# Kernel optimization log

Hardware: AMD Instinct MI355X
Metric: run time of the kernel (lower is better)

## Reference

```python
import jax, jax.numpy as jnp
import numpy as np

BATCH = 4096
INPUT_SIZE = 8192
IO = 16            # inputoutput_dim
D_STATE = 32       # statespace_dim
N_STAGES = INPUT_SIZE // IO  # 512


def _glorot(key, shape):
    # glorot-uniform over the trailing matrix dims, matching get_random_glorot_uniform_matrix
    lim = float(np.sqrt(6.0 / (shape[-2] + shape[-1])))
    return jax.random.uniform(key, shape, minval=-lim, maxval=lim, dtype=jnp.float32)


def setup_inputs() -> dict:
    key = jax.random.key(0)
    ks = jax.random.split(key, 10)
    U = jax.random.normal(ks[0], (BATCH, INPUT_SIZE), dtype=jnp.float32)
    A = _glorot(ks[1], (N_STAGES, D_STATE, D_STATE))
    B = _glorot(ks[2], (N_STAGES, D_STATE, IO))
    C = _glorot(ks[3], (N_STAGES, IO, D_STATE))
    D = _glorot(ks[4], (N_STAGES, IO, IO))
    E = _glorot(ks[5], (N_STAGES, D_STATE, D_STATE))
    F = _glorot(ks[6], (N_STAGES, D_STATE, IO))
    G = _glorot(ks[7], (N_STAGES, IO, D_STATE))
    lim_b = float(np.sqrt(6.0 / INPUT_SIZE))
    bias = jax.random.uniform(ks[8], (INPUT_SIZE,), minval=-lim_b, maxval=lim_b, dtype=jnp.float32)
    return {"U": U, "A": A, "B": B, "C": C, "D": D, "E": E, "F": F, "G": G, "bias": bias}


def reference(U, A, B, C, D, E, F, G, bias):
    bt, p = U.shape
    n, io, d = C.shape
    u = U.reshape(bt, n, io).transpose(1, 0, 2)  # (N, batch, io)
    x0 = jnp.zeros((bt, d), dtype=U.dtype)

    # causal: y_k = C_k x_k + D_k u_k ; x_{k+1} = A_k x_k + B_k u_k, x_0 = 0
    def causal_step(x, inp):
        A_k, B_k, C_k, D_k, u_k = inp
        y_k = x @ C_k.T + u_k @ D_k.T
        x = x @ A_k.T + u_k @ B_k.T
        return x, y_k

    _, y_c = jax.lax.scan(causal_step, x0, (A, B, C, D, u))

    # anticausal (runs from last stage to first): y_k += G_k z_k ; z_{k-1} = E_k z_k + F_k u_k, z_N = 0
    def anti_step(z, inp):
        E_k, F_k, G_k, u_k = inp
        y_k = z @ G_k.T
        z = z @ E_k.T + u_k @ F_k.T
        return z, y_k

    _, y_a = jax.lax.scan(anti_step, x0, (E, F, G, u), reverse=True)

    y = (y_c + y_a).transpose(1, 0, 2).reshape(bt, p) + bias
    return y
```

## Files before the change

kernel.cpp:

```cpp
#include <hip/hip_runtime.h>


#define BATCH 4096
#define NCH   16
#define CHS   32
#define SROWS (BATCH + 32)
#define TSTR  36

typedef __attribute__((ext_vector_type(8))) short short8;
typedef __attribute__((ext_vector_type(4))) float f32x4;
typedef short8 __attribute__((may_alias)) short8a;
typedef f32x4 __attribute__((may_alias)) f32x4a;
typedef unsigned __attribute__((may_alias)) uinta;

#define MFMA16(a, b, c) __builtin_amdgcn_mfma_f32_16x16x32_bf16(a, b, c, 0, 0, 0)

__device__ __forceinline__ unsigned short bf16u(float x) {
  unsigned u = __builtin_bit_cast(unsigned, x);
  u += 0x7fffu + ((u >> 16) & 1u);
  return (unsigned short)(u >> 16);
}
__device__ __forceinline__ float bf2f(unsigned short u) {
  return __builtin_bit_cast(float, ((unsigned)u) << 16);
}
__device__ __forceinline__ unsigned pk2(float a, float b) {
  return (unsigned)bf16u(a) | (((unsigned)bf16u(b)) << 16);
}
template <int DT>
__device__ __forceinline__ const void* eptr(const void* b, long e) {
  return (const char*)b + e * (DT ? 4 : 2);
}

__device__ __forceinline__ void gload16(const void* g, void* lds) {
  __builtin_amdgcn_global_load_lds((const __attribute__((address_space(1))) void*)g,
                                   (__attribute__((address_space(3))) void*)lds, 16, 0, 0);
}
__device__ __forceinline__ void stage_blob8(const short* g, short* lds, int w, int lane) {
#pragma unroll
  for (int c = 0; c < 2; ++c) {
    const int ob = (w * 2 + c) * 1024;
    gload16((const char*)g + ob + lane * 16, (char*)lds + ob);
  }
}
__device__ __forceinline__ void stage_blob2k(const short* g, short* lds, int w, int lane) {
  if (w < 2) {
    const int ob = w * 1024;
    gload16((const char*)g + ob + lane * 16, (char*)lds + ob);
  }
}

template <int DT, int ROWS, int COLS, int PSTR>
__device__ __forceinline__ void stage2(const void* gp, short* hi, short* lo, int tid) {
  if constexpr (DT == 0) {
    const uinta* gu = (const uinta*)gp;
    for (int i = tid; i < ROWS * COLS / 2; i += 256) {
      int r = i / (COLS / 2), c = i - r * (COLS / 2);
      ((uinta*)(hi + r * PSTR))[c] = gu[i];
    }
  } else {
    const float* gf = (const float*)gp;
    for (int i = tid; i < ROWS * COLS; i += 256) {
      int r = i / COLS, c = i - r * COLS;
      float v = gf[i];
      unsigned short h = bf16u(v);
      hi[r * PSTR + c] = (short)h;
      lo[r * PSTR + c] = (short)bf16u(v - bf2f(h));
    }
  }
}
template <int DT, int ROWS, int COLS, int PSTR>
__device__ __forceinline__ void stage1(const void* gp, short* hi, int tid) {
  if constexpr (DT == 0) {
    const uinta* gu = (const uinta*)gp;
    for (int i = tid; i < ROWS * COLS / 2; i += 256) {
      int r = i / (COLS / 2), c = i - r * (COLS / 2);
      ((uinta*)(hi + r * PSTR))[c] = gu[i];
    }
  } else {
    const float* gf = (const float*)gp;
    for (int i = tid; i < ROWS * COLS; i += 256) {
      int r = i / COLS, c = i - r * COLS;
      hi[r * PSTR + c] = (short)bf16u(gf[i]);
    }
  }
}

__device__ __forceinline__ short8 ldfrag32(const short* l, int lane, int nbase) {
  int n = nbase + (lane & 15), q = lane >> 4;
  return *(const short8a*)(l + n * 40 + q * 8);
}
__device__ __forceinline__ short8 ldfrag16(const short* l, int lane, int nbase) {
  int n = nbase + (lane & 15), q = lane >> 4;
  short8 z = {};
  if (q < 2) z = *(const short8a*)(l + n * 24 + q * 8);
  return z;
}

__device__ __forceinline__ void twr(const f32x4* acc, float* T, int lane) {
  const int c = lane & 15, q = lane >> 4;
#pragma unroll
  for (int h = 0; h < 2; ++h)
#pragma unroll
    for (int r = 0; r < 4; ++r) T[(q * 4 + r) * TSTR + h * 16 + c] = acc[h][r];
}
__device__ __forceinline__ void trd(const float* T, int lane, short8& hi, short8& lo) {
  const int m = lane & 15, q = lane >> 4;
  const float* p = T + m * TSTR + q * 8;
#pragma unroll
  for (int j = 0; j < 8; ++j) {
    float v = p[j];
    unsigned short h = bf16u(v);
    hi[j] = (short)h;
    lo[j] = (short)bf16u(v - bf2f(h));
  }
}

template <int DT> struct URaw;
template <> struct URaw<0> { short8 s; };
template <> struct URaw<1> { f32x4 a, b; };

template <int DT>
__device__ __forceinline__ URaw<DT> ldu_raw(const void* U, size_t off) {
  URaw<DT> r;
  if constexpr (DT == 0) {
    r.s = *(const short8a*)((const short*)U + off);
  } else {
    const f32x4a* p = (const f32x4a*)((const float*)U + off);
    r.a = p[0];
    r.b = p[1];
  }
  return r;
}
template <int DT>
__device__ __forceinline__ void u_cvt(const URaw<DT>& r, short8& uhi, short8& ulo) {
  if constexpr (DT == 0) {
    uhi = r.s;
    ulo = short8{};
  } else {
#pragma unroll
    for (int j = 0; j < 4; ++j) {
      float v = r.a[j];
      unsigned short h = bf16u(v);
      uhi[j] = (short)h;
      ulo[j] = (short)bf16u(v - bf2f(h));
    }
#pragma unroll
    for (int j = 0; j < 4; ++j) {
      float v = r.b[j];
      unsigned short h = bf16u(v);
      uhi[4 + j] = (short)h;
      ulo[4 + j] = (short)bf16u(v - bf2f(h));
    }
  }
}
template <int DT, int MODE> struct UL {
  URaw<DT> r;
  __device__ __forceinline__ void fetch(const void* U, const short*, size_t row, int k, int qq) {
    r = ldu_raw<DT>(U, row * 8192 + (size_t)k * 16 + qq * 8);
  }
  __device__ __forceinline__ void get(short8& hi, short8& lo) const { u_cvt<DT>(r, hi, lo); }
};
template <> struct UL<1, 2> {
  short8 h, l;
  __device__ __forceinline__ void fetch(const void*, const short* Ub, size_t row, int k, int qq) {
    const short* p = Ub + (row * 1024 + (size_t)k * 2 + qq) * 16;
    h = *(const short8a*)p;
    l = *(const short8a*)(p + 8);
  }
  __device__ __forceinline__ void get(short8& hi, short8& lo) const { hi = h; lo = l; }
};

template <int DT>
__device__ __forceinline__ float ldbias(const void* b, int i) {
  if constexpr (DT == 0) return bf2f((unsigned short)((const short*)b)[i]);
  else return ((const float*)b)[i];
}

template <int DT>
__device__ __forceinline__ void step_state(const short8& Xhi, const short8& Xlo,
                                           const short8& uhi, const short8& ulo,
                                           const short* Mhi, const short* Mlo,
                                           const short* Bhi, const short* Blo,
                                           f32x4* out, int lane) {
#pragma unroll
  for (int h = 0; h < 2; ++h) {
    const f32x4 z4 = {0.f, 0.f, 0.f, 0.f};
    short8 bA = ldfrag32(Mhi, lane, h * 16);
    f32x4 ax = MFMA16(Xhi, bA, z4);
    ax = MFMA16(Xlo, bA, ax);
    short8 bB = ldfrag16(Bhi, lane, h * 16);
    ax = MFMA16(uhi, bB, ax);
    if constexpr (DT) {
      short8 bAl = ldfrag32(Mlo, lane, h * 16);
      ax = MFMA16(Xhi, bAl, ax);
      ax = MFMA16(ulo, bB, ax);
      short8 bBl = ldfrag16(Blo, lane, h * 16);
      ax = MFMA16(uhi, bBl, ax);
    }
    out[h] = ax;
  }
}

__global__ void k_detect(const unsigned short* __restrict__ U16, int* __restrict__ flag) {
  int lane = threadIdx.x;
  int bad = 0;
  for (int i = lane; i < 512; i += 64) {
    int e = (U16[i] >> 7) & 0xFF;
    bad += ((e > 134) || (e < 96 && e != 0)) ? 1 : 0;
  }
#pragma unroll
  for (int s = 32; s; s >>= 1) bad += __shfl_xor(bad, s);
  if (lane == 0) *flag = (bad > 48) ? 1 : 0;
}

template <int DT, int ROWS, int COLS, int PSTR, bool LO>
__device__ __forceinline__ void cvt_mat(const void* gp, short* hi, short* lo, int tid) {
  if constexpr (DT == 0) {
    const unsigned short* gs = (const unsigned short*)gp;
    for (int i = tid; i < ROWS * COLS; i += 256) {
      int r = i / COLS, c = i - r * COLS;
      hi[r * PSTR + c] = (short)gs[i];
    }
  } else {
    const float* gf = (const float*)gp;
    for (int i = tid; i < ROWS * COLS; i += 256) {
      int r = i / COLS, c = i - r * COLS;
      float v = gf[i];
      unsigned short h = bf16u(v);
      hi[r * PSTR + c] = (short)h;
      if constexpr (LO) lo[r * PSTR + c] = (short)bf16u(v - bf2f(h));
    }
  }
}
template <int DT>
__global__ __launch_bounds__(256) void k_prep(
    const int* __restrict__ flagp,
    const void* __restrict__ Am, const void* __restrict__ Bm, const void* __restrict__ Cm,
    const void* __restrict__ Dm, const void* __restrict__ Em, const void* __restrict__ Fm,
    const void* __restrict__ Gm,
    short* __restrict__ ABb, short* __restrict__ EFb, short* __restrict__ CDb,
    short* __restrict__ Gb) {
  if (*flagp != DT) return;
  const int k = blockIdx.x, tid = threadIdx.x;
  short* ab = ABb + (size_t)k * 4096;
  short* ef = EFb + (size_t)k * 4096;
  short* cd = CDb + (size_t)k * 1024;
  short* gb = Gb + (size_t)k * 1024;
  cvt_mat<DT, 32, 32, 40, true>(eptr<DT>(Am, (long)k * 1024), ab, ab + 1280, tid);
  cvt_mat<DT, 32, 16, 24, true>(eptr<DT>(Bm, (long)k * 512), ab + 2560, ab + 3328, tid);
  cvt_mat<DT, 32, 32, 40, true>(eptr<DT>(Em, (long)k * 1024), ef, ef + 1280, tid);
  cvt_mat<DT, 32, 16, 24, true>(eptr<DT>(Fm, (long)k * 512), ef + 2560, ef + 3328, tid);
  cvt_mat<DT, 16, 32, 40, false>(eptr<DT>(Cm, (long)k * 512), cd, nullptr, tid);
  cvt_mat<DT, 16, 16, 24, false>(eptr<DT>(Dm, (long)k * 256), cd + 640, nullptr, tid);
  cvt_mat<DT, 16, 32, 40, false>(eptr<DT>(Gm, (long)k * 512), gb, nullptr, tid);
}
__global__ __launch_bounds__(256) void k_prepU(const int* __restrict__ flagp,
                                               const float* __restrict__ Uf,
                                               short* __restrict__ Ub) {
  if (*flagp != 1) return;
  const size_t i = (size_t)blockIdx.x * 256 + threadIdx.x;
  const f32x4a* p = (const f32x4a*)(Uf + i * 8);
  f32x4 a = p[0], b = p[1];
  short8 hi, lo;
#pragma unroll
  for (int j = 0; j < 4; ++j) {
    unsigned short h = bf16u(a[j]);
    hi[j] = (short)h;
    lo[j] = (short)bf16u(a[j] - bf2f(h));
  }
#pragma unroll
  for (int j = 0; j < 4; ++j) {
    unsigned short h = bf16u(b[j]);
    hi[4 + j] = (short)h;
    lo[4 + j] = (short)bf16u(b[j] - bf2f(h));
  }
  *(short8a*)(Ub + i * 16) = hi;
  *(short8a*)(Ub + i * 16 + 8) = lo;
}

template <int DT, int MODE>
__global__ __launch_bounds__(256, 4) void k1_scan(
    const int* __restrict__ flagp, const void* __restrict__ U,
    const void* __restrict__ Am, const void* __restrict__ Bm,
    const void* __restrict__ Em, const void* __restrict__ Fm,
    const short* __restrict__ ABb, const short* __restrict__ EFb,
    const short* __restrict__ Ub,
    float* __restrict__ Sc, float* __restrict__ Sa) {
  if (*flagp != DT) return;
  const int ch = blockIdx.x, tile = blockIdx.y;
  const bool ident = (tile == 64);
  const int tid = threadIdx.x, lane = tid & 63, w = tid >> 6;
  const int s = ch * CHS;
  __shared__ __align__(16) short bAB[2][4096];
  __shared__ __align__(16) short bEF[2][4096];
  __shared__ __align__(16) float T[4][2][16 * TSTR];

  short8 Xhi = {}, Xlo = {}, Zhi = {}, Zlo = {};
  if (ident) {
    const int m = lane & 15, q = lane >> 4;
    short8 id = {};
#pragma unroll
    for (int j = 0; j < 8; ++j) id[j] = ((q * 8 + j) == (w * 16 + m)) ? (short)0x3F80 : (short)0;
    Xhi = id; Zhi = id;
  }

  auto stAB = [&](int k, int b) {
    if constexpr (MODE >= 1) {
      stage_blob8(ABb + (size_t)k * 4096, bAB[b], w, lane);
    } else {
      stage2<DT, 32, 32, 40>(eptr<DT>(Am, (long)k * 1024), bAB[b], bAB[b] + 1280, tid);
      stage2<DT, 32, 16, 24>(eptr<DT>(Bm, (long)k * 512), bAB[b] + 2560, bAB[b] + 3328, tid);
    }
  };
  auto stEF = [&](int k, int b) {
    if constexpr (MODE >= 1) {
      stage_blob8(EFb + (size_t)k * 4096, bEF[b], w, lane);
    } else {
      stage2<DT, 32, 32, 40>(eptr<DT>(Em, (long)k * 1024), bEF[b], bEF[b] + 1280, tid);
      stage2<DT, 32, 16, 24>(eptr<DT>(Fm, (long)k * 512), bEF[b] + 2560, bEF[b] + 3328, tid);
    }
  };

  stAB(s, 0);
  stEF(s + CHS - 1, 0);

  const size_t row = (size_t)(ident ? 0 : (tile * 64 + w * 16 + (lane & 15)));
  const int qq = (lane >> 4) & 1;
  UL<DT, MODE> upc, upa;
  if (!ident) {
    upc.fetch(U, Ub, row, s, qq);
    upa.fetch(U, Ub, row, s + CHS - 1, qq);
  }
  __syncthreads();

  f32x4 aX[2], aZ[2];
#pragma unroll 2
  for (int t = 0; t < CHS; ++t) {
    const int kc = s + t, ka = s + CHS - 1 - t, buf = t & 1;
    if (t < CHS - 1) {
      stAB(kc + 1, buf ^ 1);
      stEF(ka - 1, buf ^ 1);
    }
    short8 uch = {}, ucl = {}, uah = {}, ual = {};
    if (!ident) {
      upc.get(uch, ucl);
      upa.get(uah, ual);
      if (t < CHS - 1) {
        upc.fetch(U, Ub, row, kc + 1, qq);
        upa.fetch(U, Ub, row, ka - 1, qq);
      }
    }
    step_state<DT>(Xhi, Xlo, uch, ucl, bAB[buf], bAB[buf] + 1280, bAB[buf] + 2560,
                   bAB[buf] + 3328, aX, lane);
    step_state<DT>(Zhi, Zlo, uah, ual, bEF[buf], bEF[buf] + 1280, bEF[buf] + 2560,
                   bEF[buf] + 3328, aZ, lane);
    twr(aX, T[w][0], lane);
    twr(aZ, T[w][1], lane);
    trd(T[w][0], lane, Xhi, Xlo);
    trd(T[w][1], lane, Zhi, Zlo);
    __syncthreads();
  }

  if (!ident || w < 2) {
    const int grow = tile * 64 + w * 16;
#pragma unroll
    for (int h = 0; h < 2; ++h)
#pragma unroll
      for (int r = 0; r < 4; ++r) {
        const int m = (lane >> 4) * 4 + r, col = h * 16 + (lane & 15);
        const size_t off = ((size_t)ch * SROWS + grow + m) * 32 + col;
        Sc[off] = aX[h][r];
        Sa[off] = aZ[h][r];
      }
  }
}

__global__ __launch_bounds__(256) void k2_comb(float* __restrict__ Sc, float* __restrict__ Sa) {
  const int dir = blockIdx.y;
  const int r = threadIdx.x >> 5, j = threadIdx.x & 31;
  const int row = blockIdx.x * 8 + r;
  float* S = dir ? Sa : Sc;
  __shared__ float P[32][33];
  __shared__ float xs[8][33];
  float x = 0.f;
  for (int it = 0; it < NCH; ++it) {
    const int ch = dir ? (NCH - 1 - it) : it;
    const size_t base = ((size_t)ch * SROWS + row) * 32 + j;
    const float s_local = S[base];
    for (int i = threadIdx.x; i < 1024; i += 256)
      P[i >> 5][i & 31] = S[((size_t)ch * SROWS + BATCH + (i >> 5)) * 32 + (i & 31)];
    xs[r][j] = x;
    __syncthreads();
    S[base] = x;
    float acc = s_local;
#pragma unroll
    for (int m = 0; m < 32; ++m) acc += xs[r][m] * P[m][j];
    x = acc;
    __syncthreads();
  }
}

template <int DT, int MODE>
__global__ __launch_bounds__(256, 3) void k3_merged(
    const int* __restrict__ flagp, const void* __restrict__ U, const void* __restrict__ biasv,
    const short* __restrict__ ABb, const short* __restrict__ EFb,
    const short* __restrict__ CDb, const short* __restrict__ Gb,
    const short* __restrict__ Ub,
    const float* __restrict__ xin, const float* __restrict__ zin,
    void* __restrict__ out) {
  if (*flagp != DT) return;
  const int ch = blockIdx.x, tile = blockIdx.y;
  const int tid = threadIdx.x, lane = tid & 63, w = tid >> 6;
  const int s = ch * CHS;
  __shared__ __align__(16) short bAB[2][4096];
  __shared__ __align__(16) short bEF[2][4096];
  __shared__ __align__(16) short bCD[2][1024];
  __shared__ __align__(16) short bG[2][1024];
  __shared__ __align__(16) float T[4][16 * TSTR];

  const int cidx = lane & 15, quad = lane >> 4, qq = quad & 1;
  const size_t row = (size_t)(tile * 64 + w * 16 + cidx);

  short8 Xhi, Xlo, Zhi, Zlo;
  {
    const float* xp = xin + ((size_t)ch * SROWS + row) * 32 + quad * 8;
    const float* zp = zin + ((size_t)ch * SROWS + row) * 32 + quad * 8;
#pragma unroll
    for (int j = 0; j < 8; ++j) {
      float v = xp[j];
      unsigned short h = bf16u(v);
      Xhi[j] = (short)h;
      Xlo[j] = (short)bf16u(v - bf2f(h));
      float z = zp[j];
      unsigned short hz = bf16u(z);
      Zhi[j] = (short)hz;
      Zlo[j] = (short)bf16u(z - bf2f(hz));
    }
  }

  stage_blob8(ABb + (size_t)s * 4096, bAB[0], w, lane);
  stage_blob2k(CDb + (size_t)s * 1024, bCD[0], w, lane);
  stage_blob8(EFb + (size_t)(s + CHS - 1) * 4096, bEF[0], w, lane);
  stage_blob2k(Gb + (size_t)(s + CHS - 1) * 1024, bG[0], w, lane);
  UL<DT, MODE> upc, upa;
  upc.fetch(U, Ub, row, s, qq);
  upa.fetch(U, Ub, row, s + CHS - 1, qq);
  __syncthreads();

  f32x4 aX[2], aZ[2];
#pragma unroll 2
  for (int t = 0; t < CHS; ++t) {
    const int kc = s + t, ka = s + CHS - 1 - t, buf = t & 1;
    if (t < CHS - 1) {
      stage_blob8(ABb + (size_t)(kc + 1) * 4096, bAB[buf ^ 1], w, lane);
      stage_blob2k(CDb + (size_t)(kc + 1) * 1024, bCD[buf ^ 1], w, lane);
      stage_blob8(EFb + (size_t)(ka - 1) * 4096, bEF[buf ^ 1], w, lane);
      stage_blob2k(Gb + (size_t)(ka - 1) * 1024, bG[buf ^ 1], w, lane);
    }
    short8 uh, ul, vh, vl;
    upc.get(uh, ul);
    upa.get(vh, vl);
    if (t < CHS - 1) {
      upc.fetch(U, Ub, row, kc + 1, qq);
      upa.fetch(U, Ub, row, ka - 1, qq);
    }
    const f32x4 z4 = {0.f, 0.f, 0.f, 0.f};
    const short8 cf = ldfrag32(bCD[buf], lane, 0);
    f32x4 yc = MFMA16(Xhi, cf, z4);
    yc = MFMA16(Xlo, cf, yc);
    const short8 df = ldfrag16(bCD[buf] + 640, lane, 0);
    yc = MFMA16(uh, df, yc);
    if constexpr (DT) yc = MFMA16(ul, df, yc);
    const short8 gf = ldfrag32(bG[buf], lane, 0);
    f32x4 yz = MFMA16(Zhi, gf, z4);
    yz = MFMA16(Zlo, gf, yz);

    const float bv = ldbias<DT>(biasv, kc * 16 + cidx);
    const size_t rbase = (size_t)(tile * 64 + w * 16 + quad * 4) * 8192;
    const size_t oc = rbase + (size_t)kc * 16 + cidx;
    const size_t oa = rbase + (size_t)ka * 16 + cidx;
    if constexpr (DT == 0) {
      short* o = (short*)out;
      if (t < CHS / 2) {
#pragma unroll
        for (int r = 0; r < 4; ++r) o[oc + (size_t)r * 8192] = (short)bf16u(yc[r] + bv);
#pragma unroll
        for (int r = 0; r < 4; ++r) o[oa + (size_t)r * 8192] = (short)bf16u(yz[r]);
      } else {
#pragma unroll
        for (int r = 0; r < 4; ++r) {
          const float c = bf2f((unsigned short)o[oc + (size_t)r * 8192]);
          o[oc + (size_t)r * 8192] = (short)bf16u(c + yc[r] + bv);
        }
#pragma unroll
        for (int r = 0; r < 4; ++r) {
          const float c = bf2f((unsigned short)o[oa + (size_t)r * 8192]);
          o[oa + (size_t)r * 8192] = (short)bf16u(c + yz[r]);
        }
      }
    } else {
      float* o = (float*)out;
      if (t < CHS / 2) {
        *(uinta*)(o + oc) = pk2(yc[0] + bv, yc[1] + bv);
        *(uinta*)(o + oc + 2 * 8192) = pk2(yc[2] + bv, yc[3] + bv);
        *(uinta*)(o + oa) = pk2(yz[0], yz[1]);
        *(uinta*)(o + oa + 2 * 8192) = pk2(yz[2], yz[3]);
      } else {
        const unsigned p0 = *(const uinta*)(o + oc);
        const unsigned p1 = *(const uinta*)(o + oc + 2 * 8192);
        o[oc + 0 * 8192] = bf2f((unsigned short)(p0 & 0xffffu)) + yc[0] + bv;
        o[oc + 1 * 8192] = bf2f((unsigned short)(p0 >> 16)) + yc[1] + bv;
        o[oc + 2 * 8192] = bf2f((unsigned short)(p1 & 0xffffu)) + yc[2] + bv;
        o[oc + 3 * 8192] = bf2f((unsigned short)(p1 >> 16)) + yc[3] + bv;
        const unsigned q0 = *(const uinta*)(o + oa);
        const unsigned q1 = *(const uinta*)(o + oa + 2 * 8192);
        o[oa + 0 * 8192] = bf2f((unsigned short)(q0 & 0xffffu)) + yz[0];
        o[oa + 1 * 8192] = bf2f((unsigned short)(q0 >> 16)) + yz[1];
        o[oa + 2 * 8192] = bf2f((unsigned short)(q1 & 0xffffu)) + yz[2];
        o[oa + 3 * 8192] = bf2f((unsigned short)(q1 >> 16)) + yz[3];
      }
    }
    step_state<DT>(Xhi, Xlo, uh, ul, bAB[buf], bAB[buf] + 1280, bAB[buf] + 2560,
                   bAB[buf] + 3328, aX, lane);
    step_state<DT>(Zhi, Zlo, vh, vl, bEF[buf], bEF[buf] + 1280, bEF[buf] + 2560,
                   bEF[buf] + 3328, aZ, lane);
    twr(aX, T[w], lane);
    trd(T[w], lane, Xhi, Xlo);
    twr(aZ, T[w], lane);
    trd(T[w], lane, Zhi, Zlo);
    __syncthreads();
  }
}

template <int DT>
__global__ __launch_bounds__(256, 4) void k3_legacy(
    const int* __restrict__ flagp, const void* __restrict__ U,
    const void* __restrict__ Am, const void* __restrict__ Bm,
    const void* __restrict__ Cm, const void* __restrict__ Dm,
    const void* __restrict__ Em, const void* __restrict__ Fm,
    const void* __restrict__ Gm, const void* __restrict__ biasv,
    const float* __restrict__ xin, const float* __restrict__ zin,
    void* __restrict__ out) {
  if (*flagp != DT) return;
  const int ch = blockIdx.x, tile = blockIdx.y;
  const int tid = threadIdx.x, lane = tid & 63, w = tid >> 6;
  const int s = ch * CHS;
  __shared__ __align__(16) short bM[2][4096];
  __shared__ __align__(16) short bO[2][1024];
  __shared__ __align__(16) float T[4][16 * TSTR];
  const int cidx = lane & 15, quad = lane >> 4, qq = quad & 1;
  const size_t row = (size_t)(tile * 64 + w * 16 + cidx);

  auto stC = [&](int k, int b) {
    stage2<DT, 32, 32, 40>(eptr<DT>(Am, (long)k * 1024), bM[b], bM[b] + 1280, tid);
    stage2<DT, 32, 16, 24>(eptr<DT>(Bm, (long)k * 512), bM[b] + 2560, bM[b] + 3328, tid);
    stage1<DT, 16, 32, 40>(eptr<DT>(Cm, (long)k * 512), bO[b], tid);
    stage1<DT, 16, 16, 24>(eptr<DT>(Dm, (long)k * 256), bO[b] + 640, tid);
  };
  auto stA = [&](int k, int b) {
    stage2<DT, 32, 32, 40>(eptr<DT>(Em, (long)k * 1024), bM[b], bM[b] + 1280, tid);
    stage2<DT, 32, 16, 24>(eptr<DT>(Fm, (long)k * 512), bM[b] + 2560, bM[b] + 3328, tid);
    stage1<DT, 16, 32, 40>(eptr<DT>(Gm, (long)k * 512), bO[b], tid);
  };

  short8 Xhi, Xlo;
  {
    const float* xp = xin + ((size_t)ch * SROWS + row) * 32 + quad * 8;
#pragma unroll
    for (int j = 0; j < 8; ++j) {
      float v = xp[j];
      unsigned short h = bf16u(v);
      Xhi[j] = (short)h;
      Xlo[j] = (short)bf16u(v - bf2f(h));
    }
  }
  stC(s, 0);
  UL<DT, 0> up;
  up.fetch(U, nullptr, row, s, qq);
  __syncthreads();

  f32x4 aX[2];
#pragma unroll 2
  for (int t = 0; t < CHS; ++t) {
    const int k = s + t, buf = t & 1;
    if (t < CHS - 1) stC(k + 1, buf ^ 1);
    short8 uh, ul;
    up.get(uh, ul);
    if (t < CHS - 1) up.fetch(U, nullptr, row, k + 1, qq);
    const f32x4 z4 = {0.f, 0.f, 0.f, 0.f};
    const short8 cf = ldfrag32(bO[buf], lane, 0);
    f32x4 ya = MFMA16(Xhi, cf, z4);
    ya = MFMA16(Xlo, cf, ya);
    const short8 df = ldfrag16(bO[buf] + 640, lane, 0);
    ya = MFMA16(uh, df, ya);
    if constexpr (DT) ya = MFMA16(ul, df, ya);
    const float bv = ldbias<DT>(biasv, k * 16 + cidx);
    {
      const size_t obase = (size_t)(tile * 64 + w * 16 + quad * 4) * 8192 + (size_t)k * 16 + cidx;
      if constexpr (DT == 0) {
        short* o = (short*)out;
#pragma unroll
        for (int r = 0; r < 4; ++r) o[obase + (size_t)r * 8192] = (short)bf16u(ya[r] + bv);
      } else {
        float* o = (float*)out;
#pragma unroll
        for (int r = 0; r < 4; ++r) o[obase + (size_t)r * 8192] = ya[r] + bv;
      }
    }
    step_state<DT>(Xhi, Xlo, uh, ul, bM[buf], bM[buf] + 1280, bM[buf] + 2560, bM[buf] + 3328,
                   aX, lane);
    twr(aX, T[w], lane);
    trd(T[w], lane, Xhi, Xlo);
    __syncthreads();
  }

  short8 Zhi, Zlo;
  {
    const float* zp = zin + ((size_t)ch * SROWS + row) * 32 + quad * 8;
#pragma unroll
    for (int j = 0; j < 8; ++j) {
      float v = zp[j];
      unsigned short h = bf16u(v);
      Zhi[j] = (short)h;
      Zlo[j] = (short)bf16u(v - bf2f(h));
    }
  }
  stA(s + CHS - 1, 0);
  up.fetch(U, nullptr, row, s + CHS - 1, qq);
  __syncthreads();

  f32x4 aZ[2];
#pragma unroll 2
  for (int t = 0; t < CHS; ++t) {
    const int k = s + CHS - 1 - t, buf = t & 1;
    if (t < CHS - 1) stA(k - 1, buf ^ 1);
    short8 uh, ul;
    up.get(uh, ul);
    if (t < CHS - 1) up.fetch(U, nullptr, row, k - 1, qq);
    const f32x4 z4 = {0.f, 0.f, 0.f, 0.f};
    const short8 gf = ldfrag32(bO[buf], lane, 0);
    f32x4 ya = MFMA16(Zhi, gf, z4);
    ya = MFMA16(Zlo, gf, ya);
    {
      const size_t obase = (size_t)(tile * 64 + w * 16 + quad * 4) * 8192 + (size_t)k * 16 + cidx;
      if constexpr (DT == 0) {
        short* o = (short*)out;
#pragma unroll
        for (int r = 0; r < 4; ++r) {
          const float c = bf2f((unsigned short)o[obase + (size_t)r * 8192]);
          o[obase + (size_t)r * 8192] = (short)bf16u(c + ya[r]);
        }
      } else {
        float* o = (float*)out;
#pragma unroll
        for (int r = 0; r < 4; ++r) o[obase + (size_t)r * 8192] += ya[r];
      }
    }
    step_state<DT>(Zhi, Zlo, uh, ul, bM[buf], bM[buf] + 1280, bM[buf] + 2560, bM[buf] + 3328,
                   aZ, lane);
    twr(aZ, T[w], lane);
    trd(T[w], lane, Zhi, Zlo);
    __syncthreads();
  }
}

extern "C" void kernel_launch(void* const* d_in, const int* in_sizes, int n_in,
                              void* d_out, int out_size, void* d_ws, size_t ws_size,
                              hipStream_t stream) {
  (void)in_sizes; (void)n_in; (void)out_size;
  const void* U = d_in[0];
  const void* A = d_in[1];
  const void* B = d_in[2];
  const void* C = d_in[3];
  const void* D = d_in[4];
  const void* E = d_in[5];
  const void* F = d_in[6];
  const void* G = d_in[7];
  const void* bias = d_in[8];

  constexpr size_t SC1 = (size_t)NCH * SROWS * 32;
  constexpr size_t BLOBS = (size_t)512 * 8192 * 2 + (size_t)512 * 2048 * 2;
  constexpr size_t UBB = (size_t)BATCH * 1024 * 32;
  constexpr size_t NEED1 = 1024 + BLOBS + SC1 * 8;
  constexpr size_t NEED2 = NEED1 + UBB;
  const int mode = (ws_size >= NEED2) ? 2 : (ws_size >= NEED1 ? 1 : 0);

  char* base = (char*)d_ws;
  int* flag = (int*)base;
  short* ABb = (short*)(base + 1024);
  short* EFb = ABb + (size_t)512 * 4096;
  short* CDb = EFb + (size_t)512 * 4096;
  short* Gb = CDb + (size_t)512 * 1024;
  float* Sc = (mode >= 1) ? (float*)(Gb + (size_t)512 * 1024) : (float*)(base + 1024);
  float* Sa = Sc + SC1;
  short* Ub = (short*)(Sa + SC1);

  k_detect<<<1, 64, 0, stream>>>((const unsigned short*)U, flag);
  if (mode >= 1) {
    k_prep<0><<<512, 256, 0, stream>>>(flag, A, B, C, D, E, F, G, ABb, EFb, CDb, Gb);
    k_prep<1><<<512, 256, 0, stream>>>(flag, A, B, C, D, E, F, G, ABb, EFb, CDb, Gb);
  }
  if (mode == 2) k_prepU<<<16384, 256, 0, stream>>>(flag, (const float*)U, Ub);

  if (mode >= 1) {
    k1_scan<0, 1><<<dim3(NCH, 65), 256, 0, stream>>>(flag, U, A, B, E, F, ABb, EFb, Ub, Sc, Sa);
    if (mode == 2)
      k1_scan<1, 2><<<dim3(NCH, 65), 256, 0, stream>>>(flag, U, A, B, E, F, ABb, EFb, Ub, Sc, Sa);
    else
      k1_scan<1, 1><<<dim3(NCH, 65), 256, 0, stream>>>(flag, U, A, B, E, F, ABb, EFb, Ub, Sc, Sa);
    k2_comb<<<dim3(BATCH / 8, 2), 256, 0, stream>>>(Sc, Sa);
    k3_merged<0, 1><<<dim3(NCH, 64), 256, 0, stream>>>(flag, U, bias, ABb, EFb, CDb, Gb, Ub,
                                                       Sc, Sa, d_out);
    if (mode == 2)
      k3_merged<1, 2><<<dim3(NCH, 64), 256, 0, stream>>>(flag, U, bias, ABb, EFb, CDb, Gb, Ub,
                                                         Sc, Sa, d_out);
    else
      k3_merged<1, 1><<<dim3(NCH, 64), 256, 0, stream>>>(flag, U, bias, ABb, EFb, CDb, Gb, Ub,
                                                         Sc, Sa, d_out);
  } else {
    k1_scan<0, 0><<<dim3(NCH, 65), 256, 0, stream>>>(flag, U, A, B, E, F, ABb, EFb, Ub, Sc, Sa);
    k1_scan<1, 0><<<dim3(NCH, 65), 256, 0, stream>>>(flag, U, A, B, E, F, ABb, EFb, Ub, Sc, Sa);
    k2_comb<<<dim3(BATCH / 8, 2), 256, 0, stream>>>(Sc, Sa);
    k3_legacy<0><<<dim3(NCH, 64), 256, 0, stream>>>(flag, U, A, B, C, D, E, F, G, bias,
                                                    Sc, Sa, d_out);
    k3_legacy<1><<<dim3(NCH, 64), 256, 0, stream>>>(flag, U, A, B, C, D, E, F, G, bias,
                                                    Sc, Sa, d_out);
  }
}
```

Before: 605.4 us.

## Shrink LDS blobs, move C/D/G fragments to registers, prefetch output reads

Packs the B/F matrices at a tighter row stride (20 instead of 24 shorts), so each staged A|B blob shrinks to 3840 shorts and is loaded with a mix of 16-byte and 4-byte direct-to-LDS loads. The C/D/G output fragments are now loaded from global straight into registers one step ahead instead of being double-buffered in LDS. The scratch transpose buffer in the scan kernel is reduced to one per wave, and the merged kernel's occupancy hint rises from 3 to 4 blocks. The read-modify-write of partial outputs in the second half is prefetched one step early into registers, trading more register pressure and a possible LDS bank-conflict change for lower LDS use and shorter load latency on the critical path.

```diff
diff --git a/kernel.cpp b/kernel.cpp
--- a/kernel.cpp
+++ b/kernel.cpp
@@ -35,17 +35,21 @@
   __builtin_amdgcn_global_load_lds((const __attribute__((address_space(1))) void*)g,
                                    (__attribute__((address_space(3))) void*)lds, 16, 0, 0);
 }
-__device__ __forceinline__ void stage_blob8(const short* g, short* lds, int w, int lane) {
-#pragma unroll
-  for (int c = 0; c < 2; ++c) {
-    const int ob = (w * 2 + c) * 1024;
-    gload16((const char*)g + ob + lane * 16, (char*)lds + ob);
-  }
-}
-__device__ __forceinline__ void stage_blob2k(const short* g, short* lds, int w, int lane) {
-  if (w < 2) {
-    const int ob = w * 1024;
-    gload16((const char*)g + ob + lane * 16, (char*)lds + ob);
+__device__ __forceinline__ void gload4(const void* g, void* lds) {
+  __builtin_amdgcn_global_load_lds((const __attribute__((address_space(1))) void*)g,
+                                   (__attribute__((address_space(3))) void*)lds, 4, 0, 0);
+}
+__device__ __forceinline__ void stage_blob75(const short* g, short* lds, int w, int lane) {
+  if (w < 3) {
+#pragma unroll
+    for (int c = 0; c < 2; ++c) {
+      const int ob = (w * 2 + c) * 1024;
+      gload16((const char*)g + ob + lane * 16, (char*)lds + ob);
+    }
+  } else {
+    gload16((const char*)g + 6144 + lane * 16, (char*)lds + 6144);
+    gload4((const char*)g + 7168 + lane * 4, (char*)lds + 7168);
+    gload4((const char*)g + 7424 + lane * 4, (char*)lds + 7424);
   }
 }
 
@@ -89,10 +93,11 @@
   int n = nbase + (lane & 15), q = lane >> 4;
   return *(const short8a*)(l + n * 40 + q * 8);
 }
+template <int PSTR>
 __device__ __forceinline__ short8 ldfrag16(const short* l, int lane, int nbase) {
   int n = nbase + (lane & 15), q = lane >> 4;
   short8 z = {};
-  if (q < 2) z = *(const short8a*)(l + n * 24 + q * 8);
+  if (q < 2) z = *(const short8a*)(l + n * PSTR + q * 8);
   return z;
 }
 
@@ -176,7 +181,7 @@
   else return ((const float*)b)[i];
 }
 
-template <int DT>
+template <int DT, int BSTR>
 __device__ __forceinline__ void step_state(const short8& Xhi, const short8& Xlo,
                                            const short8& uhi, const short8& ulo,
                                            const short* Mhi, const short* Mlo,
@@ -188,13 +193,13 @@
     short8 bA = ldfrag32(Mhi, lane, h * 16);
     f32x4 ax = MFMA16(Xhi, bA, z4);
     ax = MFMA16(Xlo, bA, ax);
-    short8 bB = ldfrag16(Bhi, lane, h * 16);
+    short8 bB = ldfrag16<BSTR>(Bhi, lane, h * 16);
     ax = MFMA16(uhi, bB, ax);
     if constexpr (DT) {
       short8 bAl = ldfrag32(Mlo, lane, h * 16);
       ax = MFMA16(Xhi, bAl, ax);
       ax = MFMA16(ulo, bB, ax);
-      short8 bBl = ldfrag16(Blo, lane, h * 16);
+      short8 bBl = ldfrag16<BSTR>(Blo, lane, h * 16);
       ax = MFMA16(uhi, bBl, ax);
     }
     out[h] = ax;
@@ -247,9 +252,9 @@
   short* cd = CDb + (size_t)k * 1024;
   short* gb = Gb + (size_t)k * 1024;
   cvt_mat<DT, 32, 32, 40, true>(eptr<DT>(Am, (long)k * 1024), ab, ab + 1280, tid);
-  cvt_mat<DT, 32, 16, 24, true>(eptr<DT>(Bm, (long)k * 512), ab + 2560, ab + 3328, tid);
+  cvt_mat<DT, 32, 16, 20, true>(eptr<DT>(Bm, (long)k * 512), ab + 2560, ab + 3200, tid);
   cvt_mat<DT, 32, 32, 40, true>(eptr<DT>(Em, (long)k * 1024), ef, ef + 1280, tid);
-  cvt_mat<DT, 32, 16, 24, true>(eptr<DT>(Fm, (long)k * 512), ef + 2560, ef + 3328, tid);
+  cvt_mat<DT, 32, 16, 20, true>(eptr<DT>(Fm, (long)k * 512), ef + 2560, ef + 3200, tid);
   cvt_mat<DT, 16, 32, 40, false>(eptr<DT>(Cm, (long)k * 512), cd, nullptr, tid);
   cvt_mat<DT, 16, 16, 24, false>(eptr<DT>(Dm, (long)k * 256), cd + 640, nullptr, tid);
   cvt_mat<DT, 16, 32, 40, false>(eptr<DT>(Gm, (long)k * 512), gb, nullptr, tid);
@@ -287,13 +292,16 @@
     const short* __restrict__ Ub,
     float* __restrict__ Sc, float* __restrict__ Sa) {
   if (*flagp != DT) return;
+  constexpr int ABSZ = (MODE >= 1) ? 3840 : 4096;
+  constexpr int BLO = (MODE >= 1) ? 3200 : 3328;
+  constexpr int BSTR = (MODE >= 1) ? 20 : 24;
   const int ch = blockIdx.x, tile = blockIdx.y;
   const bool ident = (tile == 64);
   const int tid = threadIdx.x, lane = tid & 63, w = tid >> 6;
   const int s = ch * CHS;
-  __shared__ __align__(16) short bAB[2][4096];
-  __shared__ __align__(16) short bEF[2][4096];
-  __shared__ __align__(16) float T[4][2][16 * TSTR];
+  __shared__ __align__(16) short bAB[2][ABSZ];
+  __shared__ __align__(16) short bEF[2][ABSZ];
+  __shared__ __align__(16) float T[4][16 * TSTR];
 
   short8 Xhi = {}, Xlo = {}, Zhi = {}, Zlo = {};
   if (ident) {
@@ -306,7 +314,7 @@
 
   auto stAB = [&](int k, int b) {
     if constexpr (MODE >= 1) {
-      stage_blob8(ABb + (size_t)k * 4096, bAB[b], w, lane);
+      stage_blob75(ABb + (size_t)k * 4096, bAB[b], w, lane);
     } else {
       stage2<DT, 32, 32, 40>(eptr<DT>(Am, (long)k * 1024), bAB[b], bAB[b] + 1280, tid);
       stage2<DT, 32, 16, 24>(eptr<DT>(Bm, (long)k * 512), bAB[b] + 2560, bAB[b] + 3328, tid);
@@ -314,7 +322,7 @@
   };
   auto stEF = [&](int k, int b) {
     if constexpr (MODE >= 1) {
-      stage_blob8(EFb + (size_t)k * 4096, bEF[b], w, lane);
+      stage_blob75(EFb + (size_t)k * 4096, bEF[b], w, lane);
     } else {
       stage2<DT, 32, 32, 40>(eptr<DT>(Em, (long)k * 1024), bEF[b], bEF[b] + 1280, tid);
       stage2<DT, 32, 16, 24>(eptr<DT>(Fm, (long)k * 512), bEF[b] + 2560, bEF[b] + 3328, tid);
@@ -350,14 +358,14 @@
         upa.fetch(U, Ub, row, ka - 1, qq);
       }
     }
-    step_state<DT>(Xhi, Xlo, uch, ucl, bAB[buf], bAB[buf] + 1280, bAB[buf] + 2560,
-                   bAB[buf] + 3328, aX, lane);
-    step_state<DT>(Zhi, Zlo, uah, ual, bEF[buf], bEF[buf] + 1280, bEF[buf] + 2560,
-                   bEF[buf] + 3328, aZ, lane);
-    twr(aX, T[w][0], lane);
-    twr(aZ, T[w][1], lane);
-    trd(T[w][0], lane, Xhi, Xlo);
-    trd(T[w][1], lane, Zhi, Zlo);
+    step_state<DT, BSTR>(Xhi, Xlo, uch, ucl, bAB[buf], bAB[buf] + 1280, bAB[buf] + 2560,
+                         bAB[buf] + BLO, aX, lane);
+    step_state<DT, BSTR>(Zhi, Zlo, uah, ual, bEF[buf], bEF[buf] + 1280, bEF[buf] + 2560,
+                         bEF[buf] + BLO, aZ, lane);
+    twr(aX, T[w], lane);
+    trd(T[w], lane, Xhi, Xlo);
+    twr(aZ, T[w], lane);
+    trd(T[w], lane, Zhi, Zlo);
     __syncthreads();
   }
 
@@ -401,7 +409,7 @@
 }
 
 template <int DT, int MODE>
-__global__ __launch_bounds__(256, 3) void k3_merged(
+__global__ __launch_bounds__(256, 4) void k3_merged(
     const int* __restrict__ flagp, const void* __restrict__ U, const void* __restrict__ biasv,
     const short* __restrict__ ABb, const short* __restrict__ EFb,
     const short* __restrict__ CDb, const short* __restrict__ Gb,
@@ -412,10 +420,8 @@
   const int ch = blockIdx.x, tile = blockIdx.y;
   const int tid = threadIdx.x, lane = tid & 63, w = tid >> 6;
   const int s = ch * CHS;
-  __shared__ __align__(16) short bAB[2][4096];
-  __shared__ __align__(16) short bEF[2][4096];
-  __shared__ __align__(16) short bCD[2][1024];
-  __shared__ __align__(16) short bG[2][1024];
+  __shared__ __align__(16) short bAB[2][3840];
+  __shared__ __align__(16) short bEF[2][3840];
   __shared__ __align__(16) float T[4][16 * TSTR];
 
   const int cidx = lane & 15, quad = lane >> 4, qq = quad & 1;
@@ -438,13 +444,19 @@
     }
   }
 
-  stage_blob8(ABb + (size_t)s * 4096, bAB[0], w, lane);
-  stage_blob2k(CDb + (size_t)s * 1024, bCD[0], w, lane);
-  stage_blob8(EFb + (size_t)(s + CHS - 1) * 4096, bEF[0], w, lane);
-  stage_blob2k(Gb + (size_t)(s + CHS - 1) * 1024, bG[0], w, lane);
+  stage_blob75(ABb + (size_t)s * 4096, bAB[0], w, lane);
+  stage_blob75(EFb + (size_t)(s + CHS - 1) * 4096, bEF[0], w, lane);
   UL<DT, MODE> upc, upa;
   upc.fetch(U, Ub, row, s, qq);
   upa.fetch(U, Ub, row, s + CHS - 1, qq);
+  short8 cfr, dfr = {}, gfr;
+  {
+    const short* cdk = CDb + (size_t)s * 1024;
+    cfr = *(const short8a*)(cdk + cidx * 40 + quad * 8);
+    if (quad < 2) dfr = *(const short8a*)(cdk + 640 + cidx * 24 + quad * 8);
+    gfr = *(const short8a*)(Gb + (size_t)(s + CHS - 1) * 1024 + cidx * 40 + quad * 8);
+  }
+  unsigned rp0 = 0, rp1 = 0, rq0 = 0, rq1 = 0;
   __syncthreads();
 
   f32x4 aX[2], aZ[2];
@@ -452,10 +464,8 @@
   for (int t = 0; t < CHS; ++t) {
     const int kc = s + t, ka = s + CHS - 1 - t, buf = t & 1;
     if (t < CHS - 1) {
-      stage_blob8(ABb + (size_t)(kc + 1) * 4096, bAB[buf ^ 1], w, lane);
-      stage_blob2k(CDb + (size_t)(kc + 1) * 1024, bCD[buf ^ 1], w, lane);
-      stage_blob8(EFb + (size_t)(ka - 1) * 4096, bEF[buf ^ 1], w, lane);
-      stage_blob2k(Gb + (size_t)(ka - 1) * 1024, bG[buf ^ 1], w, lane);
+      stage_blob75(ABb + (size_t)(kc + 1) * 4096, bAB[buf ^ 1], w, lane);
+      stage_blob75(EFb + (size_t)(ka - 1) * 4096, bEF[buf ^ 1], w, lane);
     }
     short8 uh, ul, vh, vl;
     upc.get(uh, ul);
@@ -465,15 +475,20 @@
       upa.fetch(U, Ub, row, ka - 1, qq);
     }
     const f32x4 z4 = {0.f, 0.f, 0.f, 0.f};
-    const short8 cf = ldfrag32(bCD[buf], lane, 0);
-    f32x4 yc = MFMA16(Xhi, cf, z4);
-    yc = MFMA16(Xlo, cf, yc);
-    const short8 df = ldfrag16(bCD[buf] + 640, lane, 0);
-    yc = MFMA16(uh, df, yc);
-    if constexpr (DT) yc = MFMA16(ul, df, yc);
-    const short8 gf = ldfrag32(bG[buf], lane, 0);
-    f32x4 yz = MFMA16(Zhi, gf, z4);
-    yz = MFMA16(Zlo, gf, yz);
+    f32x4 yc = MFMA16(Xhi, cfr, z4);
+    yc = MFMA16(Xlo, cfr, yc);
+    yc = MFMA16(uh, dfr, yc);
+    if constexpr (DT) yc = MFMA16(ul, dfr, yc);
+    f32x4 yz = MFMA16(Zhi, gfr, z4);
+    yz = MFMA16(Zlo, gfr, yz);
+    if (t < CHS - 1) {
+      const short* cdk = CDb + (size_t)(kc + 1) * 1024;
+      short8 ncf = *(const short8a*)(cdk + cidx * 40 + quad * 8);
+      short8 ndf = {};
+      if (quad < 2) ndf = *(const short8a*)(cdk + 640 + cidx * 24 + quad * 8);
+      short8 ngf = *(const short8a*)(Gb + (size_t)(ka - 1) * 1024 + cidx * 40 + quad * 8);
+      cfr = ncf; dfr = ndf; gfr = ngf;
+    }
 
     const float bv = ldbias<DT>(biasv, kc * 16 + cidx);
     const size_t rbase = (size_t)(tile * 64 + w * 16 + quad * 4) * 8192;
@@ -506,24 +521,28 @@
         *(uinta*)(o + oa) = pk2(yz[0], yz[1]);
         *(uinta*)(o + oa + 2 * 8192) = pk2(yz[2], yz[3]);
       } else {
-        const unsigned p0 = *(const uinta*)(o + oc);
-        const unsigned p1 = *(const uinta*)(o + oc + 2 * 8192);
-        o[oc + 0 * 8192] = bf2f((unsigned short)(p0 & 0xffffu)) + yc[0] + bv;
-        o[oc + 1 * 8192] = bf2f((unsigned short)(p0 >> 16)) + yc[1] + bv;
-        o[oc + 2 * 8192] = bf2f((unsigned short)(p1 & 0xffffu)) + yc[2] + bv;
-        o[oc + 3 * 8192] = bf2f((unsigned short)(p1 >> 16)) + yc[3] + bv;
-        const unsigned q0 = *(const uinta*)(o + oa);
-        const unsigned q1 = *(const uinta*)(o + oa + 2 * 8192);
-        o[oa + 0 * 8192] = bf2f((unsigned short)(q0 & 0xffffu)) + yz[0];
-        o[oa + 1 * 8192] = bf2f((unsigned short)(q0 >> 16)) + yz[1];
-        o[oa + 2 * 8192] = bf2f((unsigned short)(q1 & 0xffffu)) + yz[2];
-        o[oa + 3 * 8192] = bf2f((unsigned short)(q1 >> 16)) + yz[3];
+        o[oc + 0 * 8192] = bf2f((unsigned short)(rp0 & 0xffffu)) + yc[0] + bv;
+        o[oc + 1 * 8192] = bf2f((unsigned short)(rp0 >> 16)) + yc[1] + bv;
+        o[oc + 2 * 8192] = bf2f((unsigned short)(rp1 & 0xffffu)) + yc[2] + bv;
+        o[oc + 3 * 8192] = bf2f((unsigned short)(rp1 >> 16)) + yc[3] + bv;
+        o[oa + 0 * 8192] = bf2f((unsigned short)(rq0 & 0xffffu)) + yz[0];
+        o[oa + 1 * 8192] = bf2f((unsigned short)(rq0 >> 16)) + yz[1];
+        o[oa + 2 * 8192] = bf2f((unsigned short)(rq1 & 0xffffu)) + yz[2];
+        o[oa + 3 * 8192] = bf2f((unsigned short)(rq1 >> 16)) + yz[3];
       }
-    }
-    step_state<DT>(Xhi, Xlo, uh, ul, bAB[buf], bAB[buf] + 1280, bAB[buf] + 2560,
-                   bAB[buf] + 3328, aX, lane);
-    step_state<DT>(Zhi, Zlo, vh, vl, bEF[buf], bEF[buf] + 1280, bEF[buf] + 2560,
-                   bEF[buf] + 3328, aZ, lane);
+      if (t + 1 >= CHS / 2 && t < CHS - 1) {
+        const size_t oc1 = rbase + (size_t)(kc + 1) * 16 + cidx;
+        const size_t oa1 = rbase + (size_t)(ka - 1) * 16 + cidx;
+        rp0 = *(const uinta*)(o + oc1);
+        rp1 = *(const uinta*)(o + oc1 + 2 * 8192);
+        rq0 = *(const uinta*)(o + oa1);
+        rq1 = *(const uinta*)(o + oa1 + 2 * 8192);
+      }
+    }
+    step_state<DT, 20>(Xhi, Xlo, uh, ul, bAB[buf], bAB[buf] + 1280, bAB[buf] + 2560,
+                       bAB[buf] + 3200, aX, lane);
+    step_state<DT, 20>(Zhi, Zlo, vh, vl, bEF[buf], bEF[buf] + 1280, bEF[buf] + 2560,
+                       bEF[buf] + 3200, aZ, lane);
     twr(aX, T[w], lane);
     trd(T[w], lane, Xhi, Xlo);
     twr(aZ, T[w], lane);
@@ -591,7 +610,7 @@
     const short8 cf = ldfrag32(bO[buf], lane, 0);
     f32x4 ya = MFMA16(Xhi, cf, z4);
     ya = MFMA16(Xlo, cf, ya);
-    const short8 df = ldfrag16(bO[buf] + 640, lane, 0);
+    const short8 df = ldfrag16<24>(bO[buf] + 640, lane, 0);
     ya = MFMA16(uh, df, ya);
     if constexpr (DT) ya = MFMA16(ul, df, ya);
     const float bv = ldbias<DT>(biasv, k * 16 + cidx);
@@ -607,8 +626,8 @@
         for (int r = 0; r < 4; ++r) o[obase + (size_t)r * 8192] = ya[r] + bv;
       }
     }
-    step_state<DT>(Xhi, Xlo, uh, ul, bM[buf], bM[buf] + 1280, bM[buf] + 2560, bM[buf] + 3328,
-                   aX, lane);
+    step_state<DT, 24>(Xhi, Xlo, uh, ul, bM[buf], bM[buf] + 1280, bM[buf] + 2560,
+                       bM[buf] + 3328, aX, lane);
     twr(aX, T[w], lane);
     trd(T[w], lane, Xhi, Xlo);
     __syncthreads();
@@ -656,8 +675,8 @@
         for (int r = 0; r < 4; ++r) o[obase + (size_t)r * 8192] += ya[r];
       }
     }
-    step_state<DT>(Zhi, Zlo, uh, ul, bM[buf], bM[buf] + 1280, bM[buf] + 2560, bM[buf] + 3328,
-                   aZ, lane);
+    step_state<DT, 24>(Zhi, Zlo, uh, ul, bM[buf], bM[buf] + 1280, bM[buf] + 2560,
+                       bM[buf] + 3328, aZ, lane);
     twr(aZ, T[w], lane);
     trd(T[w], lane, Zhi, Zlo);
     __syncthreads();
```

After: 911.7 us. 1.51x slower.
